# Performance work log

Hardware: AMD Instinct MI355X
Metric: run time of the kernel (lower is better)

The kernel has to match this reference:

```python
import jax, jax.numpy as jnp
import numpy as np

B, N, DIN, DOUT = 2048, 64, 512, 512


def setup_inputs() -> dict:
    key = jax.random.key(0)
    kx, kw, kb = jax.random.split(key, 3)
    x = jax.random.normal(kx, (B, N, DIN), dtype=jnp.float32)
    # stacked per-node Linear params (PyTorch Linear: y = x @ W.T + b)
    bound = 1.0 / np.sqrt(DIN)
    W = jax.random.uniform(kw, (N, DIN, DOUT), dtype=jnp.float32, minval=-bound, maxval=bound)
    b = jax.random.uniform(kb, (N, DOUT), dtype=jnp.float32, minval=-bound, maxval=bound)
    return {"x": x, "W": W, "b": b}


def reference(x, W, b):
    # per-node independent linear layers fused into one batched GEMM
    # x: [B, N, DIN], W: [N, DIN, DOUT], b: [N, DOUT]
    y = jnp.einsum('bni,nio->bno', x, W) + b  # [B, N, DOUT]
    # torch.cat along dim=1 of the per-node [B, DOUT] outputs == flatten node axis
    return y.reshape(x.shape[0], -1)  # [B, N*DOUT]
```

## Files before the change

### kernel.cpp

```cpp
#include <hip/hip_runtime.h>


#define NN 64
#define DIN 512
#define DOUT 512
#define BM 64
#define BN 256
#define BK 32
#define LDK 40
#define ROWSTRIDE (NN * DIN)
#define OUTSTRIDE (NN * DOUT)
#define KSTEPS (DIN / BK)

typedef __bf16 bf16x8 __attribute__((ext_vector_type(8)));
typedef float f32x4 __attribute__((ext_vector_type(4)));

__device__ __forceinline__ unsigned short f2bf(float f) {
    return __builtin_bit_cast(unsigned short, (__bf16)f);
}
__device__ __forceinline__ unsigned int f2bf2(float a, float b) {
    return (unsigned int)f2bf(a) | ((unsigned int)f2bf(b) << 16);
}

typedef const __attribute__((address_space(1))) unsigned int* gas1_t;
typedef __attribute__((address_space(3))) unsigned int* las3_t;
__device__ __forceinline__ void gload_lds16(const void* g, void* l) {
    __builtin_amdgcn_global_load_lds((gas1_t)g, (las3_t)l, 16, 0, 0);
}

__global__ void wt_transpose_kernel(const float* __restrict__ W,
                                    unsigned short* __restrict__ Wt) {
    __shared__ float tile[32][33];
    const int n  = blockIdx.z;
    const int i0 = blockIdx.x * 32;
    const int o0 = blockIdx.y * 32;
    const float* Wn = W + (size_t)n * DIN * DOUT;
    unsigned short* Wtn = Wt + (size_t)n * DIN * DOUT;
    const int tx = threadIdx.x, ty = threadIdx.y;
#pragma unroll
    for (int q = 0; q < 4; ++q)
        tile[ty + q * 8][tx] = Wn[(size_t)(i0 + ty + q * 8) * DOUT + (o0 + tx)];
    __syncthreads();
#pragma unroll
    for (int q = 0; q < 4; ++q)
        Wtn[(size_t)(o0 + ty + q * 8) * DIN + (i0 + tx)] = f2bf(tile[tx][ty + q * 8]);
}

__global__ __launch_bounds__(256) void node_gemm_kernel(
    const float* __restrict__ X, const unsigned short* __restrict__ Wt,
    const float* __restrict__ Bias, float* __restrict__ Out) {
    __shared__ unsigned short As[2][BM * LDK];
    __shared__ unsigned short Bs[2][BN * BK];

    const int bid = blockIdx.x;
    const int swz = (bid & 7) * 512 + (bid >> 3);
    const int node  = swz >> 6;
    const int rem   = swz & 63;
    const int mtile = rem >> 1;
    const int ntile = rem & 1;
    const int brow = mtile * BM;
    const int bcol = ntile * BN;

    const int tid  = threadIdx.x;
    const int lane = tid & 63;
    const int w    = tid >> 6;

    const float* Xb = X + (size_t)brow * ROWSTRIDE + node * DIN;
    const unsigned short* Wb = Wt + (size_t)node * DIN * DOUT + (size_t)bcol * DIN;

    const int b_rl = lane >> 2;
    const int b_cs = lane & 3;

    const int a_r = tid >> 2;
    const int a_c = tid & 3;

    const int arow = lane & 15;
    const int akk  = lane >> 4;
    const int aoff = arow * LDK + akk * 8;
    const int obase = w * 64 + (lane & 15);
    const int bswz  = akk ^ ((obase >> 1) & 3);
    const int boff  = obase * BK + bswz * 8;

    f32x4 acc[4][4] = {};
    float4 av0, av1;

    auto stageB = [&](int buf, int k0) {
#pragma unroll
        for (int q = 0; q < 4; ++q) {
            const int cb = q * 4 + w;
            const int r  = cb * 16 + b_rl;
            const int c  = b_cs ^ ((r >> 1) & 3);
            gload_lds16(Wb + (size_t)r * DIN + k0 + c * 8, &Bs[buf][cb * 512]);
        }
    };
    auto loadA = [&](int k0) {
        const float* p = Xb + (size_t)a_r * ROWSTRIDE + k0 + a_c * 8;
        av0 = *reinterpret_cast<const float4*>(p);
        av1 = *reinterpret_cast<const float4*>(p + 4);
    };
    auto storeA = [&](int buf) {
        uint4 pk;
        pk.x = f2bf2(av0.x, av0.y);
        pk.y = f2bf2(av0.z, av0.w);
        pk.z = f2bf2(av1.x, av1.y);
        pk.w = f2bf2(av1.z, av1.w);
        *reinterpret_cast<uint4*>(&As[buf][a_r * LDK + a_c * 8]) = pk;
    };

    loadA(0);
    stageB(0, 0);
    storeA(0);
    __syncthreads();

    int buf = 0;
    for (int kt = 0; kt < KSTEPS; ++kt) {
        const bool more = (kt < KSTEPS - 1);
        if (more) {
            stageB(buf ^ 1, (kt + 1) * BK);
            loadA((kt + 1) * BK);
        }
        bf16x8 af[4], bq[4];
#pragma unroll
        for (int m = 0; m < 4; ++m)
            af[m] = *reinterpret_cast<const bf16x8*>(&As[buf][aoff + m * 16 * LDK]);
#pragma unroll
        for (int n = 0; n < 4; ++n)
            bq[n] = *reinterpret_cast<const bf16x8*>(&Bs[buf][boff + n * 16 * BK]);
#pragma unroll
        for (int m = 0; m < 4; ++m)
#pragma unroll
            for (int n = 0; n < 4; ++n)
                acc[m][n] = __builtin_amdgcn_mfma_f32_16x16x32_bf16(af[m], bq[n], acc[m][n], 0, 0, 0);
        if (more) storeA(buf ^ 1);
        __syncthreads();
        buf ^= 1;
    }

    const float* bn = Bias + node * DOUT + bcol;
    float* outb = Out + (size_t)brow * OUTSTRIDE + node * DOUT + bcol;
#pragma unroll
    for (int n = 0; n < 4; ++n) {
        const int col = w * 64 + n * 16 + (lane & 15);
        const float bias = bn[col];
#pragma unroll
        for (int m = 0; m < 4; ++m) {
            const int r0 = m * 16 + akk * 4;
#pragma unroll
            for (int j = 0; j < 4; ++j)
                outb[(size_t)(r0 + j) * OUTSTRIDE + col] = acc[m][n][j] + bias;
        }
    }
}

extern "C" void kernel_launch(void* const* d_in, const int* in_sizes, int n_in,
                              void* d_out, int out_size, void* d_ws, size_t ws_size,
                              hipStream_t stream) {
    const float* x = (const float*)d_in[0];
    const float* W = (const float*)d_in[1];
    const float* b = (const float*)d_in[2];
    float* out = (float*)d_out;
    unsigned short* Wt = (unsigned short*)d_ws;

    wt_transpose_kernel<<<dim3(DIN / 32, DOUT / 32, NN), dim3(32, 8), 0, stream>>>(W, Wt);
    node_gemm_kernel<<<dim3(4096), dim3(256), 0, stream>>>(x, Wt, b, out);
}
```

Before: 235.4 us.

## Stream fp32 X tiles directly to LDS and use a three-stage async pipeline

Activation tiles are now staged into LDS as fp32 through direct global-to-LDS loads with an XOR swizzle, and the bf16 conversion moves to after the LDS read. This drops the register round trip and the separate store phase for A. The double buffer becomes a triple buffer: two tiles are prefetched ahead, and manual vmcnt waits plus raw barriers take the place of __syncthreads. In exchange, LDS use roughly doubles (fp32 A over three stages), which may reduce occupancy, and the conversion work now happens in the compute phase.

```diff
diff --git a/kernel.cpp b/kernel.cpp
--- a/kernel.cpp
+++ b/kernel.cpp
@@ -7,13 +7,13 @@
 #define BM 64
 #define BN 256
 #define BK 32
-#define LDK 40
+#define KSTEPS (DIN / BK)
 #define ROWSTRIDE (NN * DIN)
 #define OUTSTRIDE (NN * DOUT)
-#define KSTEPS (DIN / BK)
 
 typedef __bf16 bf16x8 __attribute__((ext_vector_type(8)));
 typedef float f32x4 __attribute__((ext_vector_type(4)));
+typedef unsigned int u32x4 __attribute__((ext_vector_type(4)));
 
 __device__ __forceinline__ unsigned short f2bf(float f) {
     return __builtin_bit_cast(unsigned short, (__bf16)f);
@@ -49,8 +49,8 @@
 __global__ __launch_bounds__(256) void node_gemm_kernel(
     const float* __restrict__ X, const unsigned short* __restrict__ Wt,
     const float* __restrict__ Bias, float* __restrict__ Out) {
-    __shared__ unsigned short As[2][BM * LDK];
-    __shared__ unsigned short Bs[2][BN * BK];
+    __shared__ float          As[3][BM * BK];
+    __shared__ unsigned short Bs[3][BN * BK];
 
     const int bid = blockIdx.x;
     const int swz = (bid & 7) * 512 + (bid >> 3);
@@ -68,79 +68,88 @@
     const float* Xb = X + (size_t)brow * ROWSTRIDE + node * DIN;
     const unsigned short* Wb = Wt + (size_t)node * DIN * DOUT + (size_t)bcol * DIN;
 
-    const int b_rl = lane >> 2;
-    const int b_cs = lane & 3;
-
-    const int a_r = tid >> 2;
-    const int a_c = tid & 3;
+    const float* asrc[2];
+#pragma unroll
+    for (int q = 0; q < 2; ++q) {
+        const int c = (q * 4 + w) * 64 + lane;
+        const int row = c >> 3, slot = c & 7;
+        const int gslot = slot ^ (row & 7);
+        asrc[q] = Xb + (size_t)row * ROWSTRIDE + gslot * 4;
+    }
+    const unsigned short* bsrc[4];
+#pragma unroll
+    for (int q = 0; q < 4; ++q) {
+        const int c = (q * 4 + w) * 64 + lane;
+        const int row = c >> 2, slot = c & 3;
+        const int gslot = slot ^ ((row >> 1) & 3);
+        bsrc[q] = Wb + (size_t)row * DIN + gslot * 8;
+    }
 
     const int arow = lane & 15;
     const int akk  = lane >> 4;
-    const int aoff = arow * LDK + akk * 8;
-    const int obase = w * 64 + (lane & 15);
+    const int aswz0 = (akk * 2 + 0) ^ (arow & 7);
+    const int aswz1 = (akk * 2 + 1) ^ (arow & 7);
+    const int obase = w * 64 + arow;
     const int bswz  = akk ^ ((obase >> 1) & 3);
     const int boff  = obase * BK + bswz * 8;
 
     f32x4 acc[4][4] = {};
-    float4 av0, av1;
 
-    auto stageB = [&](int buf, int k0) {
+    auto stage = [&](int buf, int ktile) {
+        const int ke = ktile * BK;
 #pragma unroll
-        for (int q = 0; q < 4; ++q) {
-            const int cb = q * 4 + w;
-            const int r  = cb * 16 + b_rl;
-            const int c  = b_cs ^ ((r >> 1) & 3);
-            gload_lds16(Wb + (size_t)r * DIN + k0 + c * 8, &Bs[buf][cb * 512]);
-        }
-    };
-    auto loadA = [&](int k0) {
-        const float* p = Xb + (size_t)a_r * ROWSTRIDE + k0 + a_c * 8;
-        av0 = *reinterpret_cast<const float4*>(p);
-        av1 = *reinterpret_cast<const float4*>(p + 4);
-    };
-    auto storeA = [&](int buf) {
-        uint4 pk;
-        pk.x = f2bf2(av0.x, av0.y);
-        pk.y = f2bf2(av0.z, av0.w);
-        pk.z = f2bf2(av1.x, av1.y);
-        pk.w = f2bf2(av1.z, av1.w);
-        *reinterpret_cast<uint4*>(&As[buf][a_r * LDK + a_c * 8]) = pk;
+        for (int q = 0; q < 2; ++q)
+            gload_lds16(asrc[q] + ke, &As[buf][(q * 4 + w) * 256]);
+#pragma unroll
+        for (int q = 0; q < 4; ++q)
+            gload_lds16(bsrc[q] + ke, &Bs[buf][(q * 4 + w) * 512]);
     };
 
-    loadA(0);
-    stageB(0, 0);
-    storeA(0);
-    __syncthreads();
-
-    int buf = 0;
-    for (int kt = 0; kt < KSTEPS; ++kt) {
-        const bool more = (kt < KSTEPS - 1);
-        if (more) {
-            stageB(buf ^ 1, (kt + 1) * BK);
-            loadA((kt + 1) * BK);
-        }
+    auto compute = [&](int buf) {
         bf16x8 af[4], bq[4];
-#pragma unroll
-        for (int m = 0; m < 4; ++m)
-            af[m] = *reinterpret_cast<const bf16x8*>(&As[buf][aoff + m * 16 * LDK]);
 #pragma unroll
         for (int n = 0; n < 4; ++n)
             bq[n] = *reinterpret_cast<const bf16x8*>(&Bs[buf][boff + n * 16 * BK]);
+#pragma unroll
+        for (int m = 0; m < 4; ++m) {
+            const float* ab = &As[buf][(arow + m * 16) * BK];
+            f32x4 lo = *reinterpret_cast<const f32x4*>(ab + aswz0 * 4);
+            f32x4 hi = *reinterpret_cast<const f32x4*>(ab + aswz1 * 4);
+            u32x4 pk;
+            pk.x = f2bf2(lo[0], lo[1]);
+            pk.y = f2bf2(lo[2], lo[3]);
+            pk.z = f2bf2(hi[0], hi[1]);
+            pk.w = f2bf2(hi[2], hi[3]);
+            af[m] = __builtin_bit_cast(bf16x8, pk);
+        }
 #pragma unroll
         for (int m = 0; m < 4; ++m)
 #pragma unroll
             for (int n = 0; n < 4; ++n)
                 acc[m][n] = __builtin_amdgcn_mfma_f32_16x16x32_bf16(af[m], bq[n], acc[m][n], 0, 0, 0);
-        if (more) storeA(buf ^ 1);
-        __syncthreads();
-        buf ^= 1;
+    };
+
+    stage(0, 0);
+    stage(1, 1);
+
+#pragma unroll
+    for (int kt = 0; kt < KSTEPS; ++kt) {
+        if (kt < KSTEPS - 1)
+            asm volatile("s_waitcnt vmcnt(6)" ::: "memory");
+        else
+            asm volatile("s_waitcnt vmcnt(0)" ::: "memory");
+        __builtin_amdgcn_sched_barrier(0);
+        __builtin_amdgcn_s_barrier();
+        __builtin_amdgcn_sched_barrier(0);
+        if (kt + 2 < KSTEPS) stage((kt + 2) % 3, kt + 2);
+        compute(kt % 3);
     }
 
     const float* bn = Bias + node * DOUT + bcol;
     float* outb = Out + (size_t)brow * OUTSTRIDE + node * DOUT + bcol;
 #pragma unroll
     for (int n = 0; n < 4; ++n) {
-        const int col = w * 64 + n * 16 + (lane & 15);
+        const int col = w * 64 + n * 16 + arow;
         const float bias = bn[col];
 #pragma unroll
         for (int m = 0; m < 4; ++m) {
```

After: 272.9 us. 15.9% more time.

## Double GEMM block tile to 128x256 with 8 waves and XOR-swizzled A LDS

Applied to the files above, without the earlier changes.

Grows the block tile from 64x256 to 128x256 with 512 threads arranged as a 2x4 wave grid, so each B tile loaded into LDS is reused by twice as many rows. This halves the number of blocks and the total traffic for the bf16 weight tiles. It also replaces the padded A layout (LDK=40) with an XOR swizzle that matches B's, and precomputes the per-thread global source pointers. In exchange it uses more LDS per block and has fewer blocks to hide latency.

```diff
diff --git a/kernel.cpp b/kernel.cpp
--- a/kernel.cpp
+++ b/kernel.cpp
@@ -4,13 +4,12 @@
 #define NN 64
 #define DIN 512
 #define DOUT 512
-#define BM 64
+#define BM 128
 #define BN 256
 #define BK 32
-#define LDK 40
+#define KSTEPS (DIN / BK)
 #define ROWSTRIDE (NN * DIN)
 #define OUTSTRIDE (NN * DOUT)
-#define KSTEPS (DIN / BK)
 
 typedef __bf16 bf16x8 __attribute__((ext_vector_type(8)));
 typedef float f32x4 __attribute__((ext_vector_type(4)));
@@ -46,16 +45,16 @@
         Wtn[(size_t)(o0 + ty + q * 8) * DIN + (i0 + tx)] = f2bf(tile[tx][ty + q * 8]);
 }
 
-__global__ __launch_bounds__(256) void node_gemm_kernel(
+__global__ __launch_bounds__(512, 4) void node_gemm_kernel(
     const float* __restrict__ X, const unsigned short* __restrict__ Wt,
     const float* __restrict__ Bias, float* __restrict__ Out) {
-    __shared__ unsigned short As[2][BM * LDK];
+    __shared__ unsigned short As[2][BM * BK];
     __shared__ unsigned short Bs[2][BN * BK];
 
     const int bid = blockIdx.x;
-    const int swz = (bid & 7) * 512 + (bid >> 3);
-    const int node  = swz >> 6;
-    const int rem   = swz & 63;
+    const int swz = (bid & 7) * 256 + (bid >> 3);
+    const int node  = swz >> 5;
+    const int rem   = swz & 31;
     const int mtile = rem >> 1;
     const int ntile = rem & 1;
     const int brow = mtile * BM;
@@ -64,37 +63,46 @@
     const int tid  = threadIdx.x;
     const int lane = tid & 63;
     const int w    = tid >> 6;
+    const int wm   = w >> 2;
+    const int wn   = w & 3;
 
     const float* Xb = X + (size_t)brow * ROWSTRIDE + node * DIN;
     const unsigned short* Wb = Wt + (size_t)node * DIN * DOUT + (size_t)bcol * DIN;
 
-    const int b_rl = lane >> 2;
-    const int b_cs = lane & 3;
+    const int a_r  = tid >> 2;
+    const int a_s  = tid & 3;
+    const int a_sw = a_s ^ ((a_r >> 1) & 3);
+    const float* a_src = Xb + (size_t)a_r * ROWSTRIDE + a_s * 8;
+    const int a_dst = a_r * BK + a_sw * 8;
 
-    const int a_r = tid >> 2;
-    const int a_c = tid & 3;
+    const unsigned short* b_src[2];
+    int b_dst[2];
+#pragma unroll
+    for (int q = 0; q < 2; ++q) {
+        const int i = q * 8 + w;
+        const int c = i * 16 + (lane >> 2);
+        const int s = lane & 3;
+        const int gs = s ^ ((c >> 1) & 3);
+        b_src[q] = Wb + (size_t)c * DIN + gs * 8;
+        b_dst[q] = i * 512;
+    }
 
     const int arow = lane & 15;
     const int akk  = lane >> 4;
-    const int aoff = arow * LDK + akk * 8;
-    const int obase = w * 64 + (lane & 15);
-    const int bswz  = akk ^ ((obase >> 1) & 3);
-    const int boff  = obase * BK + bswz * 8;
+    const int kswz = akk ^ ((arow >> 1) & 3);
+    const int afrag = (wm * 64 + arow) * BK + kswz * 8;
+    const int bfrag = (wn * 64 + arow) * BK + kswz * 8;
 
     f32x4 acc[4][4] = {};
     float4 av0, av1;
 
-    auto stageB = [&](int buf, int k0) {
+    auto stageB = [&](int buf, int kt) {
 #pragma unroll
-        for (int q = 0; q < 4; ++q) {
-            const int cb = q * 4 + w;
-            const int r  = cb * 16 + b_rl;
-            const int c  = b_cs ^ ((r >> 1) & 3);
-            gload_lds16(Wb + (size_t)r * DIN + k0 + c * 8, &Bs[buf][cb * 512]);
-        }
+        for (int q = 0; q < 2; ++q)
+            gload_lds16(b_src[q] + kt * BK, &Bs[buf][b_dst[q]]);
     };
-    auto loadA = [&](int k0) {
-        const float* p = Xb + (size_t)a_r * ROWSTRIDE + k0 + a_c * 8;
+    auto loadA = [&](int kt) {
+        const float* p = a_src + kt * BK;
         av0 = *reinterpret_cast<const float4*>(p);
         av1 = *reinterpret_cast<const float4*>(p + 4);
     };
@@ -104,7 +112,7 @@
         pk.y = f2bf2(av0.z, av0.w);
         pk.z = f2bf2(av1.x, av1.y);
         pk.w = f2bf2(av1.z, av1.w);
-        *reinterpret_cast<uint4*>(&As[buf][a_r * LDK + a_c * 8]) = pk;
+        *reinterpret_cast<uint4*>(&As[buf][a_dst]) = pk;
     };
 
     loadA(0);
@@ -116,16 +124,16 @@
     for (int kt = 0; kt < KSTEPS; ++kt) {
         const bool more = (kt < KSTEPS - 1);
         if (more) {
-            stageB(buf ^ 1, (kt + 1) * BK);
-            loadA((kt + 1) * BK);
+            stageB(buf ^ 1, kt + 1);
+            loadA(kt + 1);
         }
         bf16x8 af[4], bq[4];
 #pragma unroll
         for (int m = 0; m < 4; ++m)
-            af[m] = *reinterpret_cast<const bf16x8*>(&As[buf][aoff + m * 16 * LDK]);
+            af[m] = *reinterpret_cast<const bf16x8*>(&As[buf][afrag + m * 16 * BK]);
 #pragma unroll
         for (int n = 0; n < 4; ++n)
-            bq[n] = *reinterpret_cast<const bf16x8*>(&Bs[buf][boff + n * 16 * BK]);
+            bq[n] = *reinterpret_cast<const bf16x8*>(&Bs[buf][bfrag + n * 16 * BK]);
 #pragma unroll
         for (int m = 0; m < 4; ++m)
 #pragma unroll
@@ -140,11 +148,11 @@
     float* outb = Out + (size_t)brow * OUTSTRIDE + node * DOUT + bcol;
 #pragma unroll
     for (int n = 0; n < 4; ++n) {
-        const int col = w * 64 + n * 16 + (lane & 15);
+        const int col = wn * 64 + n * 16 + arow;
         const float bias = bn[col];
 #pragma unroll
         for (int m = 0; m < 4; ++m) {
-            const int r0 = m * 16 + akk * 4;
+            const int r0 = wm * 64 + m * 16 + akk * 4;
 #pragma unroll
             for (int j = 0; j < 4; ++j)
                 outb[(size_t)(r0 + j) * OUTSTRIDE + col] = acc[m][n][j] + bias;
@@ -162,5 +170,5 @@
     unsigned short* Wt = (unsigned short*)d_ws;
 
     wt_transpose_kernel<<<dim3(DIN / 32, DOUT / 32, NN), dim3(32, 8), 0, stream>>>(W, Wt);
-    node_gemm_kernel<<<dim3(4096), dim3(256), 0, stream>>>(x, Wt, b, out);
+    node_gemm_kernel<<<dim3(2048), dim3(512), 0, stream>>>(x, Wt, b, out);
 }
```

Measured after the change: 202.4 us. 14.0% less time.

## Keep per-node weight slice resident in LDS and stream X directly to registers

Applied to the files above, without the earlier changes.

The GEMM kernel is restructured so each 1024-thread block loads a full 64-column slice of one node's bf16 weights into LDS once. It then sweeps all 2048 batch rows in two chunks, loading X fragments straight from global memory into registers with bf16 conversion and no LDS staging or per-k-step barriers. This drops the 4096-block grid with double-buffered A/B tiles in favour of 512 large blocks, with the node mapped per XCD for weight locality. The risk is lower X reuse across columns: each X row is now read 8 times, once per column slice, versus 2 before. The direct global loads also have no software prefetch, so latency may be exposed, and the large blocks reduce occupancy.

```diff
diff --git a/kernel.cpp b/kernel.cpp
--- a/kernel.cpp
+++ b/kernel.cpp
@@ -4,13 +4,9 @@
 #define NN 64
 #define DIN 512
 #define DOUT 512
-#define BM 64
-#define BN 256
-#define BK 32
-#define LDK 40
+#define COLS 64
 #define ROWSTRIDE (NN * DIN)
 #define OUTSTRIDE (NN * DOUT)
-#define KSTEPS (DIN / BK)
 
 typedef __bf16 bf16x8 __attribute__((ext_vector_type(8)));
 typedef float f32x4 __attribute__((ext_vector_type(4)));
@@ -20,12 +16,6 @@
 }
 __device__ __forceinline__ unsigned int f2bf2(float a, float b) {
     return (unsigned int)f2bf(a) | ((unsigned int)f2bf(b) << 16);
-}
-
-typedef const __attribute__((address_space(1))) unsigned int* gas1_t;
-typedef __attribute__((address_space(3))) unsigned int* las3_t;
-__device__ __forceinline__ void gload_lds16(const void* g, void* l) {
-    __builtin_amdgcn_global_load_lds((gas1_t)g, (las3_t)l, 16, 0, 0);
 }
 
 __global__ void wt_transpose_kernel(const float* __restrict__ W,
@@ -46,108 +36,89 @@
         Wtn[(size_t)(o0 + ty + q * 8) * DIN + (i0 + tx)] = f2bf(tile[tx][ty + q * 8]);
 }
 
-__global__ __launch_bounds__(256) void node_gemm_kernel(
+__global__ __launch_bounds__(1024) void node_gemm_kernel(
     const float* __restrict__ X, const unsigned short* __restrict__ Wt,
     const float* __restrict__ Bias, float* __restrict__ Out) {
-    __shared__ unsigned short As[2][BM * LDK];
-    __shared__ unsigned short Bs[2][BN * BK];
+    __shared__ uint4 Wl[COLS * 64];
 
-    const int bid = blockIdx.x;
-    const int swz = (bid & 7) * 512 + (bid >> 3);
-    const int node  = swz >> 6;
-    const int rem   = swz & 63;
-    const int mtile = rem >> 1;
-    const int ntile = rem & 1;
-    const int brow = mtile * BM;
-    const int bcol = ntile * BN;
+    const int bid  = blockIdx.x;
+    const int xcd  = bid & 7;
+    const int seq  = bid >> 3;
+    const int node = xcd + (seq >> 3) * 8;
+    const int bcol = (seq & 7) * COLS;
 
     const int tid  = threadIdx.x;
     const int lane = tid & 63;
     const int w    = tid >> 6;
 
-    const float* Xb = X + (size_t)brow * ROWSTRIDE + node * DIN;
     const unsigned short* Wb = Wt + (size_t)node * DIN * DOUT + (size_t)bcol * DIN;
-
-    const int b_rl = lane >> 2;
-    const int b_cs = lane & 3;
-
-    const int a_r = tid >> 2;
-    const int a_c = tid & 3;
-
-    const int arow = lane & 15;
-    const int akk  = lane >> 4;
-    const int aoff = arow * LDK + akk * 8;
-    const int obase = w * 64 + (lane & 15);
-    const int bswz  = akk ^ ((obase >> 1) & 3);
-    const int boff  = obase * BK + bswz * 8;
-
-    f32x4 acc[4][4] = {};
-    float4 av0, av1;
-
-    auto stageB = [&](int buf, int k0) {
 #pragma unroll
-        for (int q = 0; q < 4; ++q) {
-            const int cb = q * 4 + w;
-            const int r  = cb * 16 + b_rl;
-            const int c  = b_cs ^ ((r >> 1) & 3);
-            gload_lds16(Wb + (size_t)r * DIN + k0 + c * 8, &Bs[buf][cb * 512]);
-        }
-    };
-    auto loadA = [&](int k0) {
-        const float* p = Xb + (size_t)a_r * ROWSTRIDE + k0 + a_c * 8;
-        av0 = *reinterpret_cast<const float4*>(p);
-        av1 = *reinterpret_cast<const float4*>(p + 4);
-    };
-    auto storeA = [&](int buf) {
-        uint4 pk;
-        pk.x = f2bf2(av0.x, av0.y);
-        pk.y = f2bf2(av0.z, av0.w);
-        pk.z = f2bf2(av1.x, av1.y);
-        pk.w = f2bf2(av1.z, av1.w);
-        *reinterpret_cast<uint4*>(&As[buf][a_r * LDK + a_c * 8]) = pk;
-    };
-
-    loadA(0);
-    stageB(0, 0);
-    storeA(0);
+    for (int i = 0; i < 4; ++i) {
+        const int s   = i * 1024 + tid;
+        const int col = s >> 6;
+        const int ks  = s & 63;
+        Wl[col * 64 + (ks ^ (col & 7))] =
+            *reinterpret_cast<const uint4*>(Wb + (size_t)col * DIN + ks * 8);
+    }
     __syncthreads();
 
-    int buf = 0;
-    for (int kt = 0; kt < KSTEPS; ++kt) {
-        const bool more = (kt < KSTEPS - 1);
-        if (more) {
-            stageB(buf ^ 1, (kt + 1) * BK);
-            loadA((kt + 1) * BK);
-        }
-        bf16x8 af[4], bq[4];
+    const int frow = lane & 15;
+    const int q    = lane >> 4;
+    const int cxor = frow & 7;
+
+    const float* Xbase = X + (size_t)(w * 64 + frow) * ROWSTRIDE + node * DIN + q * 8;
+
+    int bslot[4];
 #pragma unroll
-        for (int m = 0; m < 4; ++m)
-            af[m] = *reinterpret_cast<const bf16x8*>(&As[buf][aoff + m * 16 * LDK]);
-#pragma unroll
-        for (int n = 0; n < 4; ++n)
-            bq[n] = *reinterpret_cast<const bf16x8*>(&Bs[buf][boff + n * 16 * BK]);
-#pragma unroll
-        for (int m = 0; m < 4; ++m)
-#pragma unroll
-            for (int n = 0; n < 4; ++n)
-                acc[m][n] = __builtin_amdgcn_mfma_f32_16x16x32_bf16(af[m], bq[n], acc[m][n], 0, 0, 0);
-        if (more) storeA(buf ^ 1);
-        __syncthreads();
-        buf ^= 1;
-    }
+    for (int n = 0; n < 4; ++n) bslot[n] = (n * 16 + frow) * 64;
 
     const float* bn = Bias + node * DOUT + bcol;
-    float* outb = Out + (size_t)brow * OUTSTRIDE + node * DOUT + bcol;
+
+    for (int c = 0; c < 2; ++c) {
+        f32x4 acc[4][4] = {};
+        const float* Xc = Xbase + (size_t)c * 1024 * ROWSTRIDE;
+
 #pragma unroll
-    for (int n = 0; n < 4; ++n) {
-        const int col = w * 64 + n * 16 + (lane & 15);
-        const float bias = bn[col];
+        for (int kt = 0; kt < 16; ++kt) {
+            bf16x8 bq[4];
 #pragma unroll
-        for (int m = 0; m < 4; ++m) {
-            const int r0 = m * 16 + akk * 4;
+            for (int n = 0; n < 4; ++n) {
+                const uint4 v = Wl[bslot[n] + ((kt * 4 + q) ^ cxor)];
+                bq[n] = __builtin_bit_cast(bf16x8, v);
+            }
+            bf16x8 af[4];
 #pragma unroll
-            for (int j = 0; j < 4; ++j)
-                outb[(size_t)(r0 + j) * OUTSTRIDE + col] = acc[m][n][j] + bias;
+            for (int m = 0; m < 4; ++m) {
+                const float* p = Xc + (size_t)m * 16 * ROWSTRIDE + kt * 32;
+                const float4 lo = *reinterpret_cast<const float4*>(p);
+                const float4 hi = *reinterpret_cast<const float4*>(p + 4);
+                uint4 pk;
+                pk.x = f2bf2(lo.x, lo.y);
+                pk.y = f2bf2(lo.z, lo.w);
+                pk.z = f2bf2(hi.x, hi.y);
+                pk.w = f2bf2(hi.z, hi.w);
+                af[m] = __builtin_bit_cast(bf16x8, pk);
+            }
+#pragma unroll
+            for (int m = 0; m < 4; ++m)
+#pragma unroll
+                for (int n = 0; n < 4; ++n)
+                    acc[m][n] = __builtin_amdgcn_mfma_f32_16x16x32_bf16(af[m], bq[n], acc[m][n], 0, 0, 0);
+        }
+
+        const int rowbase = c * 1024 + w * 64;
+        float* outb = Out + (size_t)rowbase * OUTSTRIDE + node * DOUT + bcol;
+#pragma unroll
+        for (int n = 0; n < 4; ++n) {
+            const int col = n * 16 + frow;
+            const float bias = bn[col];
+#pragma unroll
+            for (int m = 0; m < 4; ++m) {
+                const int r0 = m * 16 + q * 4;
+#pragma unroll
+                for (int j = 0; j < 4; ++j)
+                    outb[(size_t)(r0 + j) * OUTSTRIDE + col] = acc[m][n][j] + bias;
+            }
         }
     }
 }
@@ -162,5 +133,5 @@
     unsigned short* Wt = (unsigned short*)d_ws;
 
     wt_transpose_kernel<<<dim3(DIN / 32, DOUT / 32, NN), dim3(32, 8), 0, stream>>>(W, Wt);
-    node_gemm_kernel<<<dim3(4096), dim3(256), 0, stream>>>(x, Wt, b, out);
+    node_gemm_kernel<<<dim3(512), dim3(1024), 0, stream>>>(x, Wt, b, out);
 }
```

Measured after the change: 886.7 us. 277% more time.
